# Optimization experiments

Measured on AMD Instinct MI355X. Metric: run time of the kernel, lower is better.

## Reference

```python
import jax, jax.numpy as jnp
import numpy as np

B, S, D, H = 2, 2048, 1024, 16
HD = D // H
NEG = -9e15


def setup_inputs() -> dict:
    key = jax.random.key(0)
    ks = jax.random.split(key, 4)
    x = jax.random.normal(ks[0], (B, S, D), dtype=jnp.float32)
    # causal mask, broadcastable over batch and heads
    mask = jnp.tril(jnp.ones((S, S), dtype=jnp.int32))[None, None]
    W_qkv = jax.random.normal(ks[1], (D, 3 * D), dtype=jnp.float32) * (1.0 / np.sqrt(D))
    b_qkv = jnp.zeros((3 * D,), dtype=jnp.float32)
    W_out = jax.random.normal(ks[2], (D, D), dtype=jnp.float32) * (1.0 / np.sqrt(D))
    b_out = jnp.zeros((D,), dtype=jnp.float32)
    return {"x": x, "mask": mask, "W_qkv": W_qkv, "b_qkv": b_qkv,
            "W_out": W_out, "b_out": b_out}


def reference(x, mask, W_qkv, b_qkv, W_out, b_out):
    b, s, _ = x.shape
    qkv = x @ W_qkv + b_qkv                       # [B,S,3D]
    qkv = qkv.reshape(b, s, H, 3 * HD)            # per-head interleaved qkv
    qkv = jnp.transpose(qkv, (0, 2, 1, 3))        # [B,H,S,3*HD]
    q, k, v = jnp.split(qkv, 3, axis=-1)          # each [B,H,S,HD]
    scores = jnp.einsum('bhqd,bhkd->bhqk', q, k) / np.sqrt(HD)
    scores = jnp.where(mask == 0, jnp.float32(NEG), scores)
    attn = jax.nn.softmax(scores, axis=-1)
    out = jnp.einsum('bhqk,bhkd->bhqd', attn, v)  # [B,H,S,HD]
    out = jnp.transpose(out, (0, 2, 1, 3)).reshape(b, s, H * HD)
    return out @ W_out + b_out
```

## Files before the change

### kernel.cpp

```cpp
#include <hip/hip_runtime.h>
#include <math.h>

constexpr int Bb = 2, Ss = 2048, Dd = 1024, Hh = 16, HDd = 64;

typedef __attribute__((ext_vector_type(8))) short bf16x8;
typedef __attribute__((ext_vector_type(4))) float f32x4;
typedef __attribute__((ext_vector_type(8))) unsigned short u16x8;
typedef __attribute__((ext_vector_type(4))) unsigned short u16x4;

__device__ __forceinline__ unsigned short bf16_rn(float f) {
  unsigned int u = __float_as_uint(f);
  u += 0x7fffu + ((u >> 16) & 1u);
  return (unsigned short)(u >> 16);
}
__device__ __forceinline__ float bf16_f(unsigned short h) {
  return __uint_as_float(((unsigned int)h) << 16);
}

__global__ __launch_bounds__(256) void split_f32(
    const float* __restrict__ in, unsigned short* __restrict__ hi,
    unsigned short* __restrict__ lo, int n8) {
  int i = blockIdx.x * 256 + threadIdx.x;
  if (i >= n8) return;
  const float4* p = (const float4*)in + (size_t)i * 2;
  float4 a = p[0], b = p[1];
  float v[8] = {a.x, a.y, a.z, a.w, b.x, b.y, b.z, b.w};
  u16x8 h, l;
  #pragma unroll
  for (int j = 0; j < 8; j++) {
    unsigned short hb = bf16_rn(v[j]);
    h[j] = hb;
    l[j] = bf16_rn(v[j] - bf16_f(hb));
  }
  *(u16x8*)(hi + (size_t)i * 8) = h;
  *(u16x8*)(lo + (size_t)i * 8) = l;
}

__global__ __launch_bounds__(256) void transpose_split_f32(
    const float* __restrict__ W, unsigned short* __restrict__ Thi,
    unsigned short* __restrict__ Tlo, int K, int N) {
  __shared__ float tile[32][33];
  int n0 = blockIdx.x * 32, k0 = blockIdx.y * 32;
  int t = threadIdx.x;
  #pragma unroll
  for (int p = 0; p < 4; p++) {
    int idx = t + p * 256;
    int kk = idx >> 5, nn = idx & 31;
    tile[kk][nn] = W[(size_t)(k0 + kk) * N + n0 + nn];
  }
  __syncthreads();
  #pragma unroll
  for (int p = 0; p < 4; p++) {
    int idx = t + p * 256;
    int nn = idx >> 5, kk = idx & 31;
    float v = tile[kk][nn];
    unsigned short hb = bf16_rn(v);
    size_t o = (size_t)(n0 + nn) * K + k0 + kk;
    Thi[o] = hb;
    Tlo[o] = bf16_rn(v - bf16_f(hb));
  }
}

typedef __attribute__((address_space(3))) unsigned int lds_u32;
typedef const __attribute__((address_space(1))) unsigned int glb_u32;
__device__ __forceinline__ void gload16(const void* g, void* l) {
  __builtin_amdgcn_global_load_lds((glb_u32*)g, (lds_u32*)l, 16, 0, 0);
}

__device__ __forceinline__ void syncb() {
  asm volatile("" ::: "memory");
  __builtin_amdgcn_s_barrier();
  asm volatile("" ::: "memory");
}
template<int N> __device__ __forceinline__ void wait_vmcnt() {
  if constexpr (N == 0)      asm volatile("s_waitcnt vmcnt(0)" ::: "memory");
  else if constexpr (N == 2) asm volatile("s_waitcnt vmcnt(2)" ::: "memory");
  else if constexpr (N == 4) asm volatile("s_waitcnt vmcnt(4)" ::: "memory");
  else if constexpr (N == 7) asm volatile("s_waitcnt vmcnt(7)" ::: "memory");
}

template<int BM, int BN>
__device__ __forceinline__ void gemm_core256(
    const unsigned short* __restrict__ Ahi, const unsigned short* __restrict__ Alo,
    const unsigned short* __restrict__ Bhi, const unsigned short* __restrict__ Blo,
    int KD, f32x4 (&acc)[BM / 32][BN / 64])
{
  constexpr int MF = BM / 32, NF = BN / 64;
  constexpr int NA = BM / 64, NB = BN / 64;
  constexpr int NV = NA + NB;
  constexpr int AELT = 2 * BM * 32;
  constexpr int BELT = 2 * BN * 32;
  constexpr int ALO = BM * 32, BLO = BN * 32;
  __shared__ unsigned short lds[2][AELT + BELT];

  const int tid = threadIdx.x, lane = tid & 63, wid = tid >> 6;
  const int m0 = blockIdx.y * BM, n0 = blockIdx.x * BN;
  const int wrow = wid >> 2, wcol = wid & 3;
  const int lrow = lane & 15, g = lane >> 4;

  const unsigned short* srcA[NA]; int dstA[NA];
  #pragma unroll
  for (int i = 0; i < NA; i++) {
    int gi = tid + i * 512;
    int lr = gi >> 2, s = gi & 3, gs = s ^ ((lr >> 1) & 3);
    const unsigned short* bp = (lr < BM) ? Ahi : Alo;
    int row = (lr < BM) ? lr : lr - BM;
    srcA[i] = bp + (size_t)(m0 + row) * KD + gs * 8;
    dstA[i] = (gi & ~63) * 8;
  }
  const unsigned short* srcB[NB]; int dstB[NB];
  #pragma unroll
  for (int i = 0; i < NB; i++) {
    int gi = tid + i * 512;
    int lr = gi >> 2, s = gi & 3, gs = s ^ ((lr >> 1) & 3);
    const unsigned short* bp = (lr < BN) ? Bhi : Blo;
    int row = (lr < BN) ? lr : lr - BN;
    srcB[i] = bp + (size_t)(n0 + row) * KD + gs * 8;
    dstB[i] = AELT + (gi & ~63) * 8;
  }

  int offA[MF], offB[NF];
  #pragma unroll
  for (int m = 0; m < MF; m++) {
    int row = wrow * (BM / 2) + m * 16 + lrow;
    offA[m] = row * 32 + ((g ^ ((row >> 1) & 3)) * 8);
  }
  #pragma unroll
  for (int n = 0; n < NF; n++) {
    int row = wcol * (BN / 4) + n * 16 + lrow;
    offB[n] = AELT + row * 32 + ((g ^ ((row >> 1) & 3)) * 8);
  }

  #pragma unroll
  for (int m = 0; m < MF; m++)
    #pragma unroll
    for (int n = 0; n < NF; n++) acc[m][n] = (f32x4){0.f, 0.f, 0.f, 0.f};

  const int nk = KD / 32;

  #pragma unroll
  for (int i = 0; i < NA; i++) gload16(srcA[i], &lds[0][dstA[i]]);
  #pragma unroll
  for (int i = 0; i < NB; i++) gload16(srcB[i], &lds[0][dstB[i]]);
  #pragma unroll
  for (int i = 0; i < NA; i++) gload16(srcA[i] + 32, &lds[1][dstA[i]]);
  #pragma unroll
  for (int i = 0; i < NB; i++) gload16(srcB[i] + 32, &lds[1][dstB[i]]);
  wait_vmcnt<NV>();
  syncb();

  for (int t = 0; t < nk; ++t) {
    const unsigned short* L = lds[t & 1];

    bf16x8 bh[NF], bl[NF];
    #pragma unroll
    for (int n = 0; n < NF; n++) {
      bh[n] = *(const bf16x8*)(L + offB[n]);
      bl[n] = *(const bf16x8*)(L + offB[n] + BLO);
    }
    {
      bf16x8 ah[MF / 2], al[MF / 2];
      #pragma unroll
      for (int m = 0; m < MF / 2; m++) {
        ah[m] = *(const bf16x8*)(L + offA[m]);
        al[m] = *(const bf16x8*)(L + offA[m] + ALO);
      }
      __builtin_amdgcn_s_setprio(1);
      #pragma unroll
      for (int m = 0; m < MF / 2; m++)
        #pragma unroll
        for (int n = 0; n < NF; n++) {
          acc[m][n] = __builtin_amdgcn_mfma_f32_16x16x32_bf16(ah[m], bh[n], acc[m][n], 0, 0, 0);
          acc[m][n] = __builtin_amdgcn_mfma_f32_16x16x32_bf16(ah[m], bl[n], acc[m][n], 0, 0, 0);
          acc[m][n] = __builtin_amdgcn_mfma_f32_16x16x32_bf16(al[m], bh[n], acc[m][n], 0, 0, 0);
        }
      __builtin_amdgcn_s_setprio(0);
    }
    syncb();
    {
      bf16x8 ah[MF / 2], al[MF / 2];
      #pragma unroll
      for (int m = 0; m < MF / 2; m++) {
        ah[m] = *(const bf16x8*)(L + offA[m + MF / 2]);
        al[m] = *(const bf16x8*)(L + offA[m + MF / 2] + ALO);
      }
      __builtin_amdgcn_s_setprio(1);
      #pragma unroll
      for (int m = 0; m < MF / 2; m++)
        #pragma unroll
        for (int n = 0; n < NF; n++) {
          acc[m + MF / 2][n] = __builtin_amdgcn_mfma_f32_16x16x32_bf16(ah[m], bh[n], acc[m + MF / 2][n], 0, 0, 0);
          acc[m + MF / 2][n] = __builtin_amdgcn_mfma_f32_16x16x32_bf16(ah[m], bl[n], acc[m + MF / 2][n], 0, 0, 0);
          acc[m + MF / 2][n] = __builtin_amdgcn_mfma_f32_16x16x32_bf16(al[m], bh[n], acc[m + MF / 2][n], 0, 0, 0);
        }
      __builtin_amdgcn_s_setprio(0);
    }

    if (t + 1 < nk) {
      asm volatile("s_waitcnt lgkmcnt(0)" ::: "memory");
      syncb();
      if (t + 2 < nk) {
        const int koff = (t + 2) * 32;
        unsigned short* W = lds[t & 1];
        #pragma unroll
        for (int i = 0; i < NA; i++) gload16(srcA[i] + koff, W + dstA[i]);
        #pragma unroll
        for (int i = 0; i < NB; i++) gload16(srcB[i] + koff, W + dstB[i]);
        wait_vmcnt<NV>();
      } else {
        wait_vmcnt<0>();
      }
      syncb();
    }
  }
}

__global__ __launch_bounds__(512) void gemm_qkv256(
    const unsigned short* __restrict__ Ahi, const unsigned short* __restrict__ Alo,
    const unsigned short* __restrict__ Bhi, const unsigned short* __restrict__ Blo,
    const float* __restrict__ bias,
    unsigned short* __restrict__ Qh, unsigned short* __restrict__ Ql,
    unsigned short* __restrict__ Kh, unsigned short* __restrict__ Kl,
    unsigned short* __restrict__ Vth, unsigned short* __restrict__ Vtl)
{
  f32x4 acc[8][3];
  gemm_core256<256, 192>(Ahi, Alo, Bhi, Blo, 1024, acc);

  const int tid = threadIdx.x, lane = tid & 63, wid = tid >> 6;
  const int lrow = lane & 15, g = lane >> 4;
  const int m0 = blockIdx.y * 256, n0 = blockIdx.x * 192;
  const int wrow = wid >> 2, wcol = wid & 3;
  const int bidx = m0 >> 11;
  const int sbase = (m0 & 2047) + wrow * 128 + g * 4;
  #pragma unroll
  for (int n = 0; n < 3; n++) {
    int gcol = n0 + wcol * 48 + n * 16 + lrow;
    unsigned hh = (unsigned)gcol / 192u;
    int inner = gcol - (int)hh * 192;
    int part = inner >> 6;
    int d = inner & 63;
    float bv = bias[gcol];
    size_t base = (size_t)(bidx * 16 + (int)hh) * 131072;
    #pragma unroll
    for (int m = 0; m < 8; m++) {
      f32x4 a = acc[m][n];
      int s0 = sbase + m * 16;
      if (part == 0) {
        #pragma unroll
        for (int r = 0; r < 4; r++) {
          float v = (a[r] + bv) * 0.18033688011112042f;
          unsigned short hi = bf16_rn(v);
          size_t ix = base + (size_t)(s0 + r) * 64 + d;
          Qh[ix] = hi; Ql[ix] = bf16_rn(v - bf16_f(hi));
        }
      } else if (part == 1) {
        #pragma unroll
        for (int r = 0; r < 4; r++) {
          float v = a[r] + bv;
          unsigned short hi = bf16_rn(v);
          size_t ix = base + (size_t)(s0 + r) * 64 + d;
          Kh[ix] = hi; Kl[ix] = bf16_rn(v - bf16_f(hi));
        }
      } else {
        u16x4 hv, lv;
        #pragma unroll
        for (int r = 0; r < 4; r++) {
          float v = a[r] + bv;
          hv[r] = bf16_rn(v);
          lv[r] = bf16_rn(v - bf16_f(hv[r]));
        }
        size_t ix = base + (size_t)d * 2048 + s0;
        *(u16x4*)(Vth + ix) = hv;
        *(u16x4*)(Vtl + ix) = lv;
      }
    }
  }
}

__global__ __launch_bounds__(512) void gemm_out256(
    const unsigned short* __restrict__ Ahi, const unsigned short* __restrict__ Alo,
    const unsigned short* __restrict__ Bhi, const unsigned short* __restrict__ Blo,
    const float* __restrict__ bias, float* __restrict__ C)
{
  f32x4 acc[4][2];
  gemm_core256<128, 128>(Ahi, Alo, Bhi, Blo, 1024, acc);

  const int tid = threadIdx.x, lane = tid & 63, wid = tid >> 6;
  const int lrow = lane & 15, g = lane >> 4;
  const int m0 = blockIdx.y * 128, n0 = blockIdx.x * 128;
  const int wrow = wid >> 2, wcol = wid & 3;
  #pragma unroll
  for (int n = 0; n < 2; n++) {
    int gcol = n0 + wcol * 32 + n * 16 + lrow;
    float bv = bias[gcol];
    #pragma unroll
    for (int m = 0; m < 4; m++) {
      f32x4 a = acc[m][n];
      #pragma unroll
      for (int r = 0; r < 4; r++) {
        int grow = m0 + wrow * 64 + m * 16 + g * 4 + r;
        C[(size_t)grow * 1024 + gcol] = a[r] + bv;
      }
    }
  }
}

__global__ __launch_bounds__(512) void flash_attn_mfma(
    const unsigned short* __restrict__ Qh, const unsigned short* __restrict__ Ql,
    const unsigned short* __restrict__ Kh, const unsigned short* __restrict__ Kl,
    const unsigned short* __restrict__ Vth, const unsigned short* __restrict__ Vtl,
    unsigned short* __restrict__ atthi, unsigned short* __restrict__ attlo)
{
  const int pidx = blockIdx.x;
  const int h = blockIdx.y, b = blockIdx.z;
  const int bh = b * Hh + h;
  const int NT = Ss / 128;
  const int qtA = pidx, qtB = NT - 1 - pidx;
  const int tid = threadIdx.x, lane = tid & 63, wid = tid >> 6;
  const int q0w = (wid < 4) ? (qtA * 128 + wid * 32)
                            : (qtB * 128 + (wid - 4) * 32);
  const int lrow = lane & 15, lg = lane >> 4;

  __shared__ unsigned short KH[2][4096], KL[2][4096];
  __shared__ unsigned short VH[4096], VL[4096];
  __shared__ unsigned short Pbuf[8][2048];

  const size_t hb = (size_t)bh * 131072;
  const unsigned short* qhb = Qh + hb;
  const unsigned short* qlb = Ql + hb;
  const unsigned short* khb = Kh + hb;
  const unsigned short* klb = Kl + hb;
  const unsigned short* vhb = Vth + hb;
  const unsigned short* vlb = Vtl + hb;

  bf16x8 qfh[2][2], qfl[2][2];
  #pragma unroll
  for (int mi = 0; mi < 2; mi++)
    #pragma unroll
    for (int ks = 0; ks < 2; ks++) {
      int off = (q0w + mi * 16 + lrow) * 64 + ks * 32 + lg * 8;
      qfh[mi][ks] = *(const bf16x8*)(qhb + off);
      qfl[mi][ks] = *(const bf16x8*)(qlb + off);
    }

  int offK[4][2], offP[2][2];
  #pragma unroll
  for (int ci = 0; ci < 4; ci++)
    #pragma unroll
    for (int ks = 0; ks < 2; ks++) {
      int row = ci * 16 + lrow;
      offK[ci][ks] = row * 64 + (((ks * 4 + lg) ^ (row & 7)) * 8);
    }
  #pragma unroll
  for (int mi = 0; mi < 2; mi++)
    #pragma unroll
    for (int ks = 0; ks < 2; ks++) {
      int row = mi * 16 + lrow;
      offP[mi][ks] = row * 64 + (((ks * 4 + lg) ^ (row & 7)) * 8);
    }

  const int sr = tid >> 3, sg = ((tid & 7) ^ ((tid >> 3) & 7)) * 8;

  float m_[2][4], l_[2][4];
  f32x4 oacc[2][4];
  #pragma unroll
  for (int mi = 0; mi < 2; mi++)
    #pragma unroll
    for (int r = 0; r < 4; r++) { m_[mi][r] = -INFINITY; l_[mi][r] = 0.f; }
  #pragma unroll
  for (int mi = 0; mi < 2; mi++)
    #pragma unroll
    for (int di = 0; di < 4; di++) oacc[mi][di] = (f32x4){0.f, 0.f, 0.f, 0.f};

  unsigned short* Pw = Pbuf[wid];
  const int nt = 2 * (qtB + 1);

  gload16(khb + (size_t)sr * 64 + sg, KH[0] + wid * 512);
  gload16(klb + (size_t)sr * 64 + sg, KL[0] + wid * 512);

  for (int t = 0; t < nt; ++t) {
    const int kv0 = t * 64;
    const bool haveK = (t + 1 < nt);

    gload16(vhb + (size_t)sr * 2048 + kv0 + sg, VH + wid * 512);
    gload16(vlb + (size_t)sr * 2048 + kv0 + sg, VL + wid * 512);
    if (haveK) {
      const int nb = (t + 1) & 1;
      const int nk = kv0 + 64;
      gload16(khb + (size_t)(nk + sr) * 64 + sg, KH[nb] + wid * 512);
      gload16(klb + (size_t)(nk + sr) * 64 + sg, KL[nb] + wid * 512);
      wait_vmcnt<4>();
    } else {
      wait_vmcnt<2>();
    }
    syncb();

    const int cb = t & 1;
    const bool active = (kv0 <= q0w + 31);

    f32x4 sf[2][4];
    if (active) {
      const unsigned short* KHc = KH[cb];
      const unsigned short* KLc = KL[cb];

      #pragma unroll
      for (int mi = 0; mi < 2; mi++)
        #pragma unroll
        for (int ci = 0; ci < 4; ci++) sf[mi][ci] = (f32x4){0.f, 0.f, 0.f, 0.f};
      __builtin_amdgcn_s_setprio(1);
      #pragma unroll
      for (int ci = 0; ci < 4; ci++) {
        bf16x8 kh0 = *(const bf16x8*)(KHc + offK[ci][0]);
        bf16x8 kh1 = *(const bf16x8*)(KHc + offK[ci][1]);
        bf16x8 kl0 = *(const bf16x8*)(KLc + offK[ci][0]);
        bf16x8 kl1 = *(const bf16x8*)(KLc + offK[ci][1]);
        #pragma unroll
        for (int mi = 0; mi < 2; mi++) {
          f32x4 s = sf[mi][ci];
          s = __builtin_amdgcn_mfma_f32_16x16x32_bf16(qfh[mi][0], kh0, s, 0, 0, 0);
          s = __builtin_amdgcn_mfma_f32_16x16x32_bf16(qfh[mi][1], kh1, s, 0, 0, 0);
          s = __builtin_amdgcn_mfma_f32_16x16x32_bf16(qfh[mi][0], kl0, s, 0, 0, 0);
          s = __builtin_amdgcn_mfma_f32_16x16x32_bf16(qfh[mi][1], kl1, s, 0, 0, 0);
          s = __builtin_amdgcn_mfma_f32_16x16x32_bf16(qfl[mi][0], kh0, s, 0, 0, 0);
          s = __builtin_amdgcn_mfma_f32_16x16x32_bf16(qfl[mi][1], kh1, s, 0, 0, 0);
          sf[mi][ci] = s;
        }
      }
      __builtin_amdgcn_s_setprio(0);

      if (kv0 + 63 > q0w) {
        #pragma unroll
        for (int mi = 0; mi < 2; mi++)
          #pragma unroll
          for (int ci = 0; ci < 4; ci++)
            #pragma unroll
            for (int r = 0; r < 4; r++) {
              int q = q0w + mi * 16 + lg * 4 + r;
              int kv = kv0 + ci * 16 + lrow;
              if (kv > q) sf[mi][ci][r] = -1e30f;
            }
      }

      #pragma unroll
      for (int mi = 0; mi < 2; mi++)
        #pragma unroll
        for (int r = 0; r < 4; r++) {
          float mx = fmaxf(fmaxf(sf[mi][0][r], sf[mi][1][r]),
                           fmaxf(sf[mi][2][r], sf[mi][3][r]));
          mx = fmaxf(mx, __shfl_xor(mx, 1));
          mx = fmaxf(mx, __shfl_xor(mx, 2));
          mx = fmaxf(mx, __shfl_xor(mx, 4));
          mx = fmaxf(mx, __shfl_xor(mx, 8));
          float mn = fmaxf(m_[mi][r], mx);
          float alpha = __builtin_amdgcn_exp2f(m_[mi][r] - mn);
          m_[mi][r] = mn;
          float rs = 0.f;
          #pragma unroll
          for (int ci = 0; ci < 4; ci++) {
            float p = __builtin_amdgcn_exp2f(sf[mi][ci][r] - mn);
            sf[mi][ci][r] = p;
            rs += p;
          }
          rs += __shfl_xor(rs, 1);
          rs += __shfl_xor(rs, 2);
          rs += __shfl_xor(rs, 4);
          rs += __shfl_xor(rs, 8);
          l_[mi][r] = l_[mi][r] * alpha + rs;
          #pragma unroll
          for (int di = 0; di < 4; di++) oacc[mi][di][r] *= alpha;
        }

      #pragma unroll
      for (int mi = 0; mi < 2; mi++)
        #pragma unroll
        for (int ci = 0; ci < 4; ci++) {
          int colb = ci * 16 + lrow;
          int gcol = colb >> 3, crem = colb & 7;
          #pragma unroll
          for (int r = 0; r < 4; r++) {
            int rr = mi * 16 + lg * 4 + r;
            Pw[rr * 64 + ((gcol ^ (rr & 7)) * 8) + crem] = bf16_rn(sf[mi][ci][r]);
          }
        }
    }

    if (haveK) wait_vmcnt<2>(); else wait_vmcnt<0>();
    syncb();

    if (active) {
      bf16x8 pa[2][2];
      #pragma unroll
      for (int mi = 0; mi < 2; mi++)
        #pragma unroll
        for (int ks = 0; ks < 2; ks++)
          pa[mi][ks] = *(const bf16x8*)(Pw + offP[mi][ks]);
      __builtin_amdgcn_s_setprio(1);
      #pragma unroll
      for (int di = 0; di < 4; di++) {
        bf16x8 vh0 = *(const bf16x8*)(VH + offK[di][0]);
        bf16x8 vh1 = *(const bf16x8*)(VH + offK[di][1]);
        bf16x8 vl0 = *(const bf16x8*)(VL + offK[di][0]);
        bf16x8 vl1 = *(const bf16x8*)(VL + offK[di][1]);
        #pragma unroll
        for (int mi = 0; mi < 2; mi++) {
          f32x4 o = oacc[mi][di];
          o = __builtin_amdgcn_mfma_f32_16x16x32_bf16(pa[mi][0], vh0, o, 0, 0, 0);
          o = __builtin_amdgcn_mfma_f32_16x16x32_bf16(pa[mi][1], vh1, o, 0, 0, 0);
          o = __builtin_amdgcn_mfma_f32_16x16x32_bf16(pa[mi][0], vl0, o, 0, 0, 0);
          o = __builtin_amdgcn_mfma_f32_16x16x32_bf16(pa[mi][1], vl1, o, 0, 0, 0);
          oacc[mi][di] = o;
        }
      }
      __builtin_amdgcn_s_setprio(0);
      asm volatile("s_waitcnt lgkmcnt(0)" ::: "memory");
    }
    syncb();
  }

  #pragma unroll
  for (int mi = 0; mi < 2; mi++) {
    float inv[4];
    #pragma unroll
    for (int r = 0; r < 4; r++) inv[r] = 1.f / l_[mi][r];
    #pragma unroll
    for (int di = 0; di < 4; di++) {
      f32x4 o = oacc[mi][di];
      #pragma unroll
      for (int r = 0; r < 4; r++) {
        float v = o[r] * inv[r];
        int srow = q0w + mi * 16 + lg * 4 + r;
        size_t idx = ((size_t)b * Ss + srow) * 1024 + h * 64 + di * 16 + lrow;
        unsigned short hi = bf16_rn(v);
        atthi[idx] = hi;
        attlo[idx] = bf16_rn(v - bf16_f(hi));
      }
    }
  }
}

extern "C" void kernel_launch(void* const* d_in, const int* in_sizes, int n_in,
                              void* d_out, int out_size, void* d_ws, size_t ws_size,
                              hipStream_t stream) {
  const float* x    = (const float*)d_in[0];
  const float* Wqkv = (const float*)d_in[2];
  const float* bqkv = (const float*)d_in[3];
  const float* Wout = (const float*)d_in[4];
  const float* bout = (const float*)d_in[5];
  float* out = (float*)d_out;

  char* ws = (char*)d_ws;
  unsigned short* Qh  = (unsigned short*)(ws);
  unsigned short* Ql  = (unsigned short*)(ws + 8388608);
  unsigned short* Kh  = (unsigned short*)(ws + 16777216);
  unsigned short* Kl  = (unsigned short*)(ws + 25165824);
  unsigned short* Vth = (unsigned short*)(ws + 33554432);
  unsigned short* Vtl = (unsigned short*)(ws + 41943040);
  unsigned short* atthi = (unsigned short*)(ws + 50331648);
  unsigned short* attlo = (unsigned short*)(ws + 58720256);
  unsigned short* xhi = (unsigned short*)(ws + 67108864);
  unsigned short* xlo = (unsigned short*)(ws + 75497472);
  unsigned short* wqh = (unsigned short*)(ws + 83886080);
  unsigned short* wql = (unsigned short*)(ws + 90177536);
  unsigned short* woh = (unsigned short*)(ws + 96468992);
  unsigned short* wol = (unsigned short*)(ws + 98566144);

  const int M = Bb * Ss;

  split_f32<<<(M * Dd / 8) / 256, 256, 0, stream>>>(x, xhi, xlo, M * Dd / 8);
  transpose_split_f32<<<dim3(3 * Dd / 32, Dd / 32), 256, 0, stream>>>(Wqkv, wqh, wql, Dd, 3 * Dd);
  transpose_split_f32<<<dim3(Dd / 32, Dd / 32), 256, 0, stream>>>(Wout, woh, wol, Dd, Dd);

  gemm_qkv256<<<dim3(16, 16), 512, 0, stream>>>(
      xhi, xlo, wqh, wql, bqkv, Qh, Ql, Kh, Kl, Vth, Vtl);

  flash_attn_mfma<<<dim3(Ss / 256, Hh, Bb), 512, 0, stream>>>(
      Qh, Ql, Kh, Kl, Vth, Vtl, atthi, attlo);

  gemm_out256<<<dim3(8, 32), 512, 0, stream>>>(
      atthi, attlo, woh, wol, bout, out);
}
```

Measured before the change: 312.7 us.

## Double the flash-attention KV tile from 64 to 128 keys per iteration

```diff
diff --git a/kernel.cpp b/kernel.cpp
--- a/kernel.cpp
+++ b/kernel.cpp
@@ -77,6 +77,7 @@
   else if constexpr (N == 2) asm volatile("s_waitcnt vmcnt(2)" ::: "memory");
   else if constexpr (N == 4) asm volatile("s_waitcnt vmcnt(4)" ::: "memory");
   else if constexpr (N == 7) asm volatile("s_waitcnt vmcnt(7)" ::: "memory");
+  else if constexpr (N == 8) asm volatile("s_waitcnt vmcnt(8)" ::: "memory");
 }
 
 template<int BM, int BN>
@@ -321,8 +322,8 @@
                             : (qtB * 128 + (wid - 4) * 32);
   const int lrow = lane & 15, lg = lane >> 4;
 
-  __shared__ unsigned short KH[2][4096], KL[2][4096];
-  __shared__ unsigned short VH[4096], VL[4096];
+  __shared__ unsigned short KH[2][8192], KL[2][8192];
+  __shared__ unsigned short VH[8192], VL[8192];
   __shared__ unsigned short Pbuf[8][2048];
 
   const size_t hb = (size_t)bh * 131072;
@@ -343,14 +344,26 @@
       qfl[mi][ks] = *(const bf16x8*)(qlb + off);
     }
 
-  int offK[4][2], offP[2][2];
-  #pragma unroll
-  for (int ci = 0; ci < 4; ci++)
+  int offK[8][2];
+  #pragma unroll
+  for (int ci = 0; ci < 8; ci++)
     #pragma unroll
     for (int ks = 0; ks < 2; ks++) {
       int row = ci * 16 + lrow;
       offK[ci][ks] = row * 64 + (((ks * 4 + lg) ^ (row & 7)) * 8);
     }
+  int offV[4][2][2];
+  #pragma unroll
+  for (int di = 0; di < 4; di++)
+    #pragma unroll
+    for (int c = 0; c < 2; c++)
+      #pragma unroll
+      for (int ks = 0; ks < 2; ks++) {
+        int row = di * 16 + lrow;
+        int g128 = c * 8 + ks * 4 + lg;
+        offV[di][c][ks] = row * 128 + ((g128 ^ (row & 15)) * 8);
+      }
+  int offP[2][2];
   #pragma unroll
   for (int mi = 0; mi < 2; mi++)
     #pragma unroll
@@ -359,7 +372,8 @@
       offP[mi][ks] = row * 64 + (((ks * 4 + lg) ^ (row & 7)) * 8);
     }
 
-  const int sr = tid >> 3, sg = ((tid & 7) ^ ((tid >> 3) & 7)) * 8;
+  const int kr0 = tid >> 3, kg0 = ((tid & 7) ^ (kr0 & 7)) * 8;
+  const int vr0 = tid >> 4, vg0 = ((tid & 15) ^ (vr0 & 15)) * 8;
 
   float m_[2][4], l_[2][4];
   f32x4 oacc[2][4];
@@ -373,32 +387,38 @@
     for (int di = 0; di < 4; di++) oacc[mi][di] = (f32x4){0.f, 0.f, 0.f, 0.f};
 
   unsigned short* Pw = Pbuf[wid];
-  const int nt = 2 * (qtB + 1);
-
-  gload16(khb + (size_t)sr * 64 + sg, KH[0] + wid * 512);
-  gload16(klb + (size_t)sr * 64 + sg, KL[0] + wid * 512);
+  const int nt = qtB + 1;
+
+  gload16(khb + (size_t)kr0 * 64 + kg0,        KH[0] + wid * 512);
+  gload16(khb + (size_t)(kr0 + 64) * 64 + kg0, KH[0] + 4096 + wid * 512);
+  gload16(klb + (size_t)kr0 * 64 + kg0,        KL[0] + wid * 512);
+  gload16(klb + (size_t)(kr0 + 64) * 64 + kg0, KL[0] + 4096 + wid * 512);
 
   for (int t = 0; t < nt; ++t) {
-    const int kv0 = t * 64;
+    const int kv0 = t * 128;
     const bool haveK = (t + 1 < nt);
 
-    gload16(vhb + (size_t)sr * 2048 + kv0 + sg, VH + wid * 512);
-    gload16(vlb + (size_t)sr * 2048 + kv0 + sg, VL + wid * 512);
+    gload16(vhb + (size_t)vr0 * 2048 + kv0 + vg0,        VH + wid * 512);
+    gload16(vhb + (size_t)(vr0 + 32) * 2048 + kv0 + vg0, VH + 4096 + wid * 512);
+    gload16(vlb + (size_t)vr0 * 2048 + kv0 + vg0,        VL + wid * 512);
+    gload16(vlb + (size_t)(vr0 + 32) * 2048 + kv0 + vg0, VL + 4096 + wid * 512);
     if (haveK) {
       const int nb = (t + 1) & 1;
-      const int nk = kv0 + 64;
-      gload16(khb + (size_t)(nk + sr) * 64 + sg, KH[nb] + wid * 512);
-      gload16(klb + (size_t)(nk + sr) * 64 + sg, KL[nb] + wid * 512);
+      const int nk = kv0 + 128;
+      gload16(khb + (size_t)(nk + kr0) * 64 + kg0,      KH[nb] + wid * 512);
+      gload16(khb + (size_t)(nk + kr0 + 64) * 64 + kg0, KH[nb] + 4096 + wid * 512);
+      gload16(klb + (size_t)(nk + kr0) * 64 + kg0,      KL[nb] + wid * 512);
+      gload16(klb + (size_t)(nk + kr0 + 64) * 64 + kg0, KL[nb] + 4096 + wid * 512);
+      wait_vmcnt<8>();
+    } else {
       wait_vmcnt<4>();
-    } else {
-      wait_vmcnt<2>();
     }
     syncb();
 
     const int cb = t & 1;
     const bool active = (kv0 <= q0w + 31);
 
-    f32x4 sf[2][4];
+    f32x4 sf[2][8];
     if (active) {
       const unsigned short* KHc = KH[cb];
       const unsigned short* KLc = KL[cb];
@@ -406,10 +426,10 @@
       #pragma unroll
       for (int mi = 0; mi < 2; mi++)
         #pragma unroll
-        for (int ci = 0; ci < 4; ci++) sf[mi][ci] = (f32x4){0.f, 0.f, 0.f, 0.f};
+        for (int ci = 0; ci < 8; ci++) sf[mi][ci] = (f32x4){0.f, 0.f, 0.f, 0.f};
       __builtin_amdgcn_s_setprio(1);
       #pragma unroll
-      for (int ci = 0; ci < 4; ci++) {
+      for (int ci = 0; ci < 8; ci++) {
         bf16x8 kh0 = *(const bf16x8*)(KHc + offK[ci][0]);
         bf16x8 kh1 = *(const bf16x8*)(KHc + offK[ci][1]);
         bf16x8 kl0 = *(const bf16x8*)(KLc + offK[ci][0]);
@@ -428,11 +448,11 @@
       }
       __builtin_amdgcn_s_setprio(0);
 
-      if (kv0 + 63 > q0w) {
+      if (kv0 + 127 > q0w) {
         #pragma unroll
         for (int mi = 0; mi < 2; mi++)
           #pragma unroll
-          for (int ci = 0; ci < 4; ci++)
+          for (int ci = 0; ci < 8; ci++)
             #pragma unroll
             for (int r = 0; r < 4; r++) {
               int q = q0w + mi * 16 + lg * 4 + r;
@@ -445,8 +465,9 @@
       for (int mi = 0; mi < 2; mi++)
         #pragma unroll
         for (int r = 0; r < 4; r++) {
-          float mx = fmaxf(fmaxf(sf[mi][0][r], sf[mi][1][r]),
-                           fmaxf(sf[mi][2][r], sf[mi][3][r]));
+          float mx = sf[mi][0][r];
+          #pragma unroll
+          for (int ci = 1; ci < 8; ci++) mx = fmaxf(mx, sf[mi][ci][r]);
           mx = fmaxf(mx, __shfl_xor(mx, 1));
           mx = fmaxf(mx, __shfl_xor(mx, 2));
           mx = fmaxf(mx, __shfl_xor(mx, 4));
@@ -456,7 +477,7 @@
           m_[mi][r] = mn;
           float rs = 0.f;
           #pragma unroll
-          for (int ci = 0; ci < 4; ci++) {
+          for (int ci = 0; ci < 8; ci++) {
             float p = __builtin_amdgcn_exp2f(sf[mi][ci][r] - mn);
             sf[mi][ci][r] = p;
             rs += p;
@@ -484,7 +505,7 @@
         }
     }
 
-    if (haveK) wait_vmcnt<2>(); else wait_vmcnt<0>();
+    if (haveK) wait_vmcnt<4>(); else wait_vmcnt<0>();
     syncb();
 
     if (active) {
@@ -497,10 +518,49 @@
       __builtin_amdgcn_s_setprio(1);
       #pragma unroll
       for (int di = 0; di < 4; di++) {
-        bf16x8 vh0 = *(const bf16x8*)(VH + offK[di][0]);
-        bf16x8 vh1 = *(const bf16x8*)(VH + offK[di][1]);
-        bf16x8 vl0 = *(const bf16x8*)(VL + offK[di][0]);
-        bf16x8 vl1 = *(const bf16x8*)(VL + offK[di][1]);
+        bf16x8 vh0 = *(const bf16x8*)(VH + offV[di][0][0]);
+        bf16x8 vh1 = *(const bf16x8*)(VH + offV[di][0][1]);
+        bf16x8 vl0 = *(const bf16x8*)(VL + offV[di][0][0]);
+        bf16x8 vl1 = *(const bf16x8*)(VL + offV[di][0][1]);
+        #pragma unroll
+        for (int mi = 0; mi < 2; mi++) {
+          f32x4 o = oacc[mi][di];
+          o = __builtin_amdgcn_mfma_f32_16x16x32_bf16(pa[mi][0], vh0, o, 0, 0, 0);
+          o = __builtin_amdgcn_mfma_f32_16x16x32_bf16(pa[mi][1], vh1, o, 0, 0, 0);
+          o = __builtin_amdgcn_mfma_f32_16x16x32_bf16(pa[mi][0], vl0, o, 0, 0, 0);
+          o = __builtin_amdgcn_mfma_f32_16x16x32_bf16(pa[mi][1], vl1, o, 0, 0, 0);
+          oacc[mi][di] = o;
+        }
+      }
+      __builtin_amdgcn_s_setprio(0);
+
+      asm volatile("s_waitcnt lgkmcnt(0)" ::: "memory");
+
+      #pragma unroll
+      for (int mi = 0; mi < 2; mi++)
+        #pragma unroll
+        for (int ci = 4; ci < 8; ci++) {
+          int colb = (ci - 4) * 16 + lrow;
+          int gcol = colb >> 3, crem = colb & 7;
+          #pragma unroll
+          for (int r = 0; r < 4; r++) {
+            int rr = mi * 16 + lg * 4 + r;
+            Pw[rr * 64 + ((gcol ^ (rr & 7)) * 8) + crem] = bf16_rn(sf[mi][ci][r]);
+          }
+        }
+
+      #pragma unroll
+      for (int mi = 0; mi < 2; mi++)
+        #pragma unroll
+        for (int ks = 0; ks < 2; ks++)
+          pa[mi][ks] = *(const bf16x8*)(Pw + offP[mi][ks]);
+      __builtin_amdgcn_s_setprio(1);
+      #pragma unroll
+      for (int di = 0; di < 4; di++) {
+        bf16x8 vh0 = *(const bf16x8*)(VH + offV[di][1][0]);
+        bf16x8 vh1 = *(const bf16x8*)(VH + offV[di][1][1]);
+        bf16x8 vl0 = *(const bf16x8*)(VL + offV[di][1][0]);
+        bf16x8 vl1 = *(const bf16x8*)(VL + offV[di][1][1]);
         #pragma unroll
         for (int mi = 0; mi < 2; mi++) {
           f32x4 o = oacc[mi][di];
```

After: 336.1 us. 1.07x slower.
